# Kernel optimization log

Measured on AMD Instinct MI355X. Metric: run time of the kernel, lower is better.

## Reference

```python
import jax, jax.numpy as jnp
import numpy as np

N = 8192
IN_DIM = 512
HID = 512


def setup_inputs() -> dict:
    key = jax.random.key(0)
    k1, k2, k3, k4 = jax.random.split(key, 4)
    input_features = jax.random.normal(k1, (N, IN_DIM), dtype=jnp.float32)
    # positive weighted adjacency so degrees > 0
    adjacency_matrix = jax.random.uniform(k2, (N, N), dtype=jnp.float32)
    # xavier_init: normal with std = 1/sqrt(in_dim/2)
    Wgcn1 = jax.random.normal(k3, (IN_DIM, HID), dtype=jnp.float32) * (1.0 / np.sqrt(IN_DIM / 2.0))
    bgcn1 = jnp.zeros((HID,), dtype=jnp.float32)
    Wgcn12 = jax.random.normal(k4, (HID, HID), dtype=jnp.float32) * (1.0 / np.sqrt(HID / 2.0))
    bgcn12 = jnp.zeros((HID,), dtype=jnp.float32)
    return {
        "input_features": input_features,
        "adjacency_matrix": adjacency_matrix,
        "Wgcn1": Wgcn1,
        "bgcn1": bgcn1,
        "Wgcn12": Wgcn12,
        "bgcn12": bgcn12,
    }


def reference(input_features, adjacency_matrix, Wgcn1, bgcn1, Wgcn12, bgcn12):
    # D^{-1/2} A D^{-1/2}: diag matmuls expressed as row/col elementwise scaling
    # (mathematically identical to torch.matmul(diag(d), A @ diag(d)))
    d_inv_sqrt = jnp.power(adjacency_matrix.sum(axis=1), -0.5)  # [N]
    norm_adj = d_inv_sqrt[:, None] * adjacency_matrix * d_inv_sqrt[None, :]  # [N, N]

    support = input_features @ Wgcn1            # [N, HID]
    out = norm_adj @ support + bgcn1            # [N, HID]
    out = jax.nn.relu(out)                      # dropout p=0.0 -> identity
    support = out @ Wgcn12                      # [N, HID]
    out = norm_adj @ support + bgcn12           # [N, HID]
    return out
```

## Files before the change

### kernel.cpp

```cpp
#include <hip/hip_runtime.h>
#include <stdint.h>


typedef __attribute__((ext_vector_type(8))) __bf16 bf16x8;
typedef __attribute__((ext_vector_type(4))) float f32x4;
typedef __attribute__((ext_vector_type(8))) unsigned short u16x8;

__device__ __forceinline__ unsigned short f2bf(float f) {
  union { float f; uint32_t u; } v; v.f = f;
  uint32_t u = v.u;
  return (unsigned short)((u + 0x7fffu + ((u >> 16) & 1u)) >> 16);
}

__device__ __forceinline__ float bf2f(unsigned short u) {
  union { uint32_t u; float f; } v; v.u = ((uint32_t)u) << 16; return v.f;
}

__device__ __forceinline__ void async_cp16(const void* g, void* lds) {
  auto gp = (const __attribute__((address_space(1))) uint32_t*)g;
  auto lp = (__attribute__((address_space(3))) uint32_t*)lds;
  __builtin_amdgcn_global_load_lds(gp, lp, 16, 0, 0);
}

__global__ __launch_bounds__(256) void k_rowsum_convert(
    const float* __restrict__ A, unsigned short* __restrict__ Abf,
    float* __restrict__ dvec, int ncols) {
  const int row = blockIdx.x;
  const float* arow = A + (size_t)row * ncols;
  unsigned short* orow = Abf + (size_t)row * ncols;
  float s = 0.f;
  for (int c = threadIdx.x * 4; c < ncols; c += 256 * 4) {
    float4 v = *(const float4*)(arow + c);
    s += (v.x + v.y) + (v.z + v.w);
    ushort4 o;
    o.x = f2bf(v.x); o.y = f2bf(v.y); o.z = f2bf(v.z); o.w = f2bf(v.w);
    *(ushort4*)(orow + c) = o;
  }
  #pragma unroll
  for (int off = 32; off > 0; off >>= 1) s += __shfl_down(s, off);
  __shared__ float red[4];
  if ((threadIdx.x & 63) == 0) red[threadIdx.x >> 6] = s;
  __syncthreads();
  if (threadIdx.x == 0) {
    float t = (red[0] + red[1]) + (red[2] + red[3]);
    dvec[row] = 1.0f / sqrtf(t);
  }
}

__global__ __launch_bounds__(256) void k_f32_to_bf16(
    const float* __restrict__ in, unsigned short* __restrict__ out, int n4) {
  int i = blockIdx.x * 256 + threadIdx.x;
  if (i < n4) {
    float4 v = ((const float4*)in)[i];
    ushort4 o;
    o.x = f2bf(v.x); o.y = f2bf(v.y); o.z = f2bf(v.z); o.w = f2bf(v.w);
    ((ushort4*)out)[i] = o;
  }
}

__global__ __launch_bounds__(256) void k_transpose_bf16(
    const float* __restrict__ in, unsigned short* __restrict__ out, int dim) {
  int o = blockIdx.x * 256 + threadIdx.x;
  if (o < dim * dim) {
    int k = o % dim;
    int n = o / dim;
    out[o] = f2bf(in[k * dim + n]);
  }
}

template <int MODE>
__global__ __launch_bounds__(256, 2) void gemm_bt(
    const unsigned short* __restrict__ Aop,
    const unsigned short* __restrict__ Bt,
    void* __restrict__ Cout,
    const float* __restrict__ dvec,
    const float* __restrict__ bias,
    int M, int N, int K) {
  constexpr int BM = 128, BN = 64, BK = 32;
  __shared__ unsigned short As[BM * BK];
  __shared__ unsigned short Bs[BN * BK];

  const int tid = threadIdx.x;
  const int w = tid >> 6;
  const int l = tid & 63;
  const int rowBase = blockIdx.y * BM;
  const int colBase = blockIdx.x * BN;
  const int waveM = w >> 1;
  const int waveN = w & 1;

  f32x4 acc[4][2];
  const f32x4 fz = {0.f, 0.f, 0.f, 0.f};
  #pragma unroll
  for (int m = 0; m < 4; ++m)
    #pragma unroll
    for (int n = 0; n < 2; ++n) acc[m][n] = fz;

  const int chunkRow = l >> 2;
  const int kOff = (l & 3) * 8;
  const unsigned short* gA0 = Aop + (size_t)(rowBase + w * 16 + chunkRow) * K + kOff;
  const unsigned short* gA1 = gA0 + (size_t)64 * K;
  const unsigned short* gB0 = Bt + (size_t)(colBase + w * 16 + chunkRow) * K + kOff;
  unsigned short* lA0 = As + w * 512;
  unsigned short* lA1 = As + (w + 4) * 512;
  unsigned short* lB0 = Bs + w * 512;

  const int kfrag = (l >> 4) * 8;
  const int lrow = l & 15;

  for (int k0 = 0; k0 < K; k0 += BK) {
    async_cp16(gA0 + k0, lA0);
    async_cp16(gA1 + k0, lA1);
    async_cp16(gB0 + k0, lB0);
    __syncthreads();

    bf16x8 af[4], bfr[2];
    #pragma unroll
    for (int m = 0; m < 4; ++m)
      af[m] = *(const bf16x8*)(As + (waveM * 64 + m * 16 + lrow) * BK + kfrag);
    #pragma unroll
    for (int n = 0; n < 2; ++n)
      bfr[n] = *(const bf16x8*)(Bs + (waveN * 32 + n * 16 + lrow) * BK + kfrag);

    #pragma unroll
    for (int m = 0; m < 4; ++m)
      #pragma unroll
      for (int n = 0; n < 2; ++n)
        acc[m][n] = __builtin_amdgcn_mfma_f32_16x16x32_bf16(af[m], bfr[n],
                                                            acc[m][n], 0, 0, 0);
    __syncthreads();
  }

  const int erow0 = rowBase + waveM * 64 + (l >> 4) * 4;
  const int ecol0 = colBase + waveN * 32 + (l & 15);
  #pragma unroll
  for (int m = 0; m < 4; ++m) {
    #pragma unroll
    for (int n = 0; n < 2; ++n) {
      #pragma unroll
      for (int j = 0; j < 4; ++j) {
        const int rowg = erow0 + m * 16 + j;
        const int colg = ecol0 + n * 16;
        float v = acc[m][n][j];
        if (MODE == 0) {
          v *= dvec[colg];
          ((unsigned short*)Cout)[(size_t)rowg * N + colg] = f2bf(v);
        }
      }
    }
  }
}

__global__ __launch_bounds__(256, 2) void gemm_big2(
    const unsigned short* __restrict__ Aop,
    const unsigned short* __restrict__ Bt,
    unsigned short* __restrict__ Pout,
    int M, int N, int K, int kLen) {
  constexpr int BK = 32;
  constexpr int BUF = 24576;
  __shared__ char lds[3 * BUF];

  const int tid = threadIdx.x;
  const int w = tid >> 6;
  const int l = tid & 63;

  const int id = blockIdx.x;
  const int q = id & 7, s = id >> 3;
  const int bx = s & 3;
  const int by = ((q & 1) << 4) | (s >> 2);
  const int bz = q >> 1;

  const int rowBase = by * 256;
  const int colBase = bx * 128;
  const int kBase = bz * kLen;
  const int waveM = w >> 1;
  const int waveN = w & 1;

  f32x4 acc[8][4];
  const f32x4 fz = {0.f, 0.f, 0.f, 0.f};
  #pragma unroll
  for (int m = 0; m < 8; ++m)
    #pragma unroll
    for (int n = 0; n < 4; ++n) acc[m][n] = fz;

  const int srcElem = ((l & 3) ^ ((l >> 3) & 3)) * 8;
  const unsigned short* aSrc =
      Aop + (size_t)(rowBase + w * 64 + (l >> 2)) * K + kBase + srcElem;
  const unsigned short* bSrc =
      Bt + (size_t)(colBase + w * 32 + (l >> 2)) * K + kBase + srcElem;
  const int dstA = w * 4096 + l * 16;
  const int dstB = 16384 + w * 2048 + l * 16;

#define STAGE_A(tt, bb)                                                   \
  {                                                                       \
    const size_t o = (size_t)(tt) * BK;                                   \
    async_cp16(aSrc + o, lds + (bb) + dstA);                              \
    async_cp16(aSrc + (size_t)16 * K + o, lds + (bb) + dstA + 1024);      \
    async_cp16(aSrc + (size_t)32 * K + o, lds + (bb) + dstA + 2048);      \
    async_cp16(aSrc + (size_t)48 * K + o, lds + (bb) + dstA + 3072);      \
  }
#define STAGE_B(tt, bb)                                                   \
  {                                                                       \
    const size_t o = (size_t)(tt) * BK;                                   \
    async_cp16(bSrc + o, lds + (bb) + dstB);                              \
    async_cp16(bSrc + (size_t)16 * K + o, lds + (bb) + dstB + 1024);      \
  }

  const int nt = kLen / BK;
  STAGE_A(0, 0); STAGE_B(0, 0);
  STAGE_A(1, BUF); STAGE_B(1, BUF);

  const int lrow = l & 15;
  const int kq = l >> 4;
  const int xr = (lrow >> 1) & 3;
  const int slotByte = ((kq ^ xr) << 4);
  const int aRow0 = (waveM * 128 + lrow) * 64;
  const int bRow0 = 16384 + (waveN * 64 + lrow) * 64;

  int cur = 0, nxt = BUF, fut = 2 * BUF;
  for (int t = 0; t < nt; ++t) {
    if (t == nt - 1) {
      asm volatile("s_waitcnt vmcnt(0)" ::: "memory");
    } else {
      asm volatile("s_waitcnt vmcnt(6)" ::: "memory");
    }
    __builtin_amdgcn_s_barrier();

    bf16x8 af[4], bfr[4];
    #pragma unroll
    for (int i = 0; i < 4; ++i)
      af[i] = *(const bf16x8*)(lds + cur + aRow0 + i * 16 * 64 + slotByte);
    #pragma unroll
    for (int n = 0; n < 4; ++n)
      bfr[n] = *(const bf16x8*)(lds + cur + bRow0 + n * 16 * 64 + slotByte);
    if (t + 2 < nt) STAGE_A(t + 2, fut);
    __builtin_amdgcn_s_barrier();
    __builtin_amdgcn_s_setprio(1);
    #pragma unroll
    for (int i = 0; i < 4; ++i)
      #pragma unroll
      for (int n = 0; n < 4; ++n)
        acc[i][n] = __builtin_amdgcn_mfma_f32_16x16x32_bf16(
            af[i], bfr[n], acc[i][n], 0, 0, 0);
    __builtin_amdgcn_s_setprio(0);

    bf16x8 af2[4];
    #pragma unroll
    for (int i = 0; i < 4; ++i)
      af2[i] = *(const bf16x8*)(lds + cur + aRow0 + (64 + i * 16) * 64 + slotByte);
    if (t + 2 < nt) STAGE_B(t + 2, fut);
    __builtin_amdgcn_s_barrier();
    __builtin_amdgcn_s_setprio(1);
    #pragma unroll
    for (int i = 0; i < 4; ++i)
      #pragma unroll
      for (int n = 0; n < 4; ++n)
        acc[4 + i][n] = __builtin_amdgcn_mfma_f32_16x16x32_bf16(
            af2[i], bfr[n], acc[4 + i][n], 0, 0, 0);
    __builtin_amdgcn_s_setprio(0);

    const int tmp = cur; cur = nxt; nxt = fut; fut = tmp;
  }
#undef STAGE_A
#undef STAGE_B

  unsigned short* pz = Pout + (size_t)bz * M * N;
  const int erow0 = rowBase + waveM * 128 + (l >> 4) * 4;
  const int ecol0 = colBase + waveN * 64 + (l & 15);
  #pragma unroll
  for (int m = 0; m < 8; ++m) {
    #pragma unroll
    for (int n = 0; n < 4; ++n) {
      #pragma unroll
      for (int j = 0; j < 4; ++j) {
        pz[(size_t)(erow0 + m * 16 + j) * N + ecol0 + n * 16] =
            f2bf(acc[m][n][j]);
      }
    }
  }
}

template <int MODE>
__global__ __launch_bounds__(256) void k_reduce(
    const unsigned short* __restrict__ parts,
    const float* __restrict__ dvec,
    const float* __restrict__ bias,
    void* __restrict__ outp, int M, int N) {
  const size_t MN = (size_t)M * N;
  const size_t idx = ((size_t)blockIdx.x * 256 + threadIdx.x) * 8;
  if (idx >= MN) return;
  const int row = (int)(idx / N);
  const int col = (int)(idx % N);
  const float di = dvec[row];
  float s[8] = {0, 0, 0, 0, 0, 0, 0, 0};
  #pragma unroll
  for (int z = 0; z < 4; ++z) {
    u16x8 v = *(const u16x8*)(parts + z * MN + idx);
    #pragma unroll
    for (int e = 0; e < 8; ++e) s[e] += bf2f(v[e]);
  }
  if (MODE == 1) {
    ushort4 o0, o1;
    unsigned short tmp[8];
    #pragma unroll
    for (int e = 0; e < 8; ++e) {
      float v = di * s[e] + bias[col + e];
      v = v > 0.f ? v : 0.f;
      tmp[e] = f2bf(v);
    }
    o0.x = tmp[0]; o0.y = tmp[1]; o0.z = tmp[2]; o0.w = tmp[3];
    o1.x = tmp[4]; o1.y = tmp[5]; o1.z = tmp[6]; o1.w = tmp[7];
    *(ushort4*)((unsigned short*)outp + idx) = o0;
    *(ushort4*)((unsigned short*)outp + idx + 4) = o1;
  } else {
    float4 o0, o1;
    o0.x = di * s[0] + bias[col + 0];
    o0.y = di * s[1] + bias[col + 1];
    o0.z = di * s[2] + bias[col + 2];
    o0.w = di * s[3] + bias[col + 3];
    o1.x = di * s[4] + bias[col + 4];
    o1.y = di * s[5] + bias[col + 5];
    o1.z = di * s[6] + bias[col + 6];
    o1.w = di * s[7] + bias[col + 7];
    *(float4*)((float*)outp + idx) = o0;
    *(float4*)((float*)outp + idx + 4) = o1;
  }
}

extern "C" void kernel_launch(void* const* d_in, const int* in_sizes, int n_in,
                              void* d_out, int out_size, void* d_ws, size_t ws_size,
                              hipStream_t stream) {
  const float* X  = (const float*)d_in[0];
  const float* A  = (const float*)d_in[1];
  const float* W1 = (const float*)d_in[2];
  const float* b1 = (const float*)d_in[3];
  const float* W2 = (const float*)d_in[4];
  const float* b2 = (const float*)d_in[5];
  float* out = (float*)d_out;

  constexpr int NN = 8192, IN = 512, HID = 512;
  constexpr int KSPLIT = 4;

  char* ws = (char*)d_ws;
  float* ddeg = (float*)ws;
  unsigned short* Abf = (unsigned short*)(ws + (32 << 10));
  unsigned short* W1t = Abf + (size_t)NN * NN;
  unsigned short* W2t = W1t + IN * HID;
  unsigned short* P0  = W2t + HID * HID;
  unsigned short* P1  = P0 + (size_t)NN * HID;
  unsigned short* parts = P1 + (size_t)NN * HID;

  k_rowsum_convert<<<NN, 256, 0, stream>>>(A, Abf, ddeg, NN);
  k_f32_to_bf16<<<(NN * IN / 4 + 255) / 256, 256, 0, stream>>>(X, P0, NN * IN / 4);
  k_transpose_bf16<<<(IN * HID + 255) / 256, 256, 0, stream>>>(W1, W1t, IN);
  k_transpose_bf16<<<(HID * HID + 255) / 256, 256, 0, stream>>>(W2, W2t, HID);

  gemm_bt<0><<<dim3(NN / 64, HID / 128), 256, 0, stream>>>(
      W1t, P0, P1, ddeg, nullptr, HID, NN, IN);
  gemm_big2<<<4 * (NN / 256) * KSPLIT, 256, 0, stream>>>(
      Abf, P1, parts, NN, HID, NN, NN / KSPLIT);
  k_reduce<1><<<(int)((size_t)NN * HID / 8 / 256), 256, 0, stream>>>(
      parts, ddeg, b1, P0, NN, HID);
  gemm_bt<0><<<dim3(NN / 64, HID / 128), 256, 0, stream>>>(
      W2t, P0, P1, ddeg, nullptr, HID, NN, HID);
  gemm_big2<<<4 * (NN / 256) * KSPLIT, 256, 0, stream>>>(
      Abf, P1, parts, NN, HID, NN, NN / KSPLIT);
  k_reduce<2><<<(int)((size_t)NN * HID / 8 / 256), 256, 0, stream>>>(
      parts, ddeg, b2, out, NN, HID);
}
```

Measured before the change: 278.5 us.

## Enlarge big GEMM tile to 256x256 and drop mid-loop barriers

The large adjacency GEMM moves from 256x128 block tiles to 256x256 tiles, so each wave computes 128x128 with 64 accumulators. This halves the number of times the A operand (the 8192x8192 adjacency) is streamed from memory and doubles arithmetic per LDS load. The inner loop is restructured to interleave fragment loads with four MFMA quadrants, and the intermediate barriers and priority hints are removed. In exchange it needs one block per CU with heavy register use, launches half as many blocks (256 on a GPU with 256 CUs), and removing barriers risks the async stage for t+2 overwriting a buffer that slower waves still read.

```diff
diff --git a/kernel.cpp b/kernel.cpp
--- a/kernel.cpp
+++ b/kernel.cpp
@@ -150,13 +150,13 @@
   }
 }
 
-__global__ __launch_bounds__(256, 2) void gemm_big2(
+__global__ __launch_bounds__(256, 1) void gemm_big4(
     const unsigned short* __restrict__ Aop,
     const unsigned short* __restrict__ Bt,
     unsigned short* __restrict__ Pout,
     int M, int N, int K, int kLen) {
   constexpr int BK = 32;
-  constexpr int BUF = 24576;
+  constexpr int BUF = 32768;
   __shared__ char lds[3 * BUF];
 
   const int tid = threadIdx.x;
@@ -165,30 +165,30 @@
 
   const int id = blockIdx.x;
   const int q = id & 7, s = id >> 3;
-  const int bx = s & 3;
-  const int by = ((q & 1) << 4) | (s >> 2);
+  const int bx = s & 1;
+  const int by = ((q & 1) << 4) | (s >> 1);
   const int bz = q >> 1;
 
   const int rowBase = by * 256;
-  const int colBase = bx * 128;
+  const int colBase = bx * 256;
   const int kBase = bz * kLen;
-  const int waveM = w >> 1;
-  const int waveN = w & 1;
-
-  f32x4 acc[8][4];
+  const int wm = w >> 1;
+  const int wn = w & 1;
+
+  f32x4 acc[8][8];
   const f32x4 fz = {0.f, 0.f, 0.f, 0.f};
   #pragma unroll
   for (int m = 0; m < 8; ++m)
     #pragma unroll
-    for (int n = 0; n < 4; ++n) acc[m][n] = fz;
+    for (int n = 0; n < 8; ++n) acc[m][n] = fz;
 
   const int srcElem = ((l & 3) ^ ((l >> 3) & 3)) * 8;
   const unsigned short* aSrc =
       Aop + (size_t)(rowBase + w * 64 + (l >> 2)) * K + kBase + srcElem;
   const unsigned short* bSrc =
-      Bt + (size_t)(colBase + w * 32 + (l >> 2)) * K + kBase + srcElem;
+      Bt + (size_t)(colBase + w * 64 + (l >> 2)) * K + kBase + srcElem;
   const int dstA = w * 4096 + l * 16;
-  const int dstB = 16384 + w * 2048 + l * 16;
+  const int dstB = 16384 + w * 4096 + l * 16;
 
 #define STAGE_A(tt, bb)                                                   \
   {                                                                       \
@@ -203,6 +203,8 @@
     const size_t o = (size_t)(tt) * BK;                                   \
     async_cp16(bSrc + o, lds + (bb) + dstB);                              \
     async_cp16(bSrc + (size_t)16 * K + o, lds + (bb) + dstB + 1024);      \
+    async_cp16(bSrc + (size_t)32 * K + o, lds + (bb) + dstB + 2048);      \
+    async_cp16(bSrc + (size_t)48 * K + o, lds + (bb) + dstB + 3072);      \
   }
 
   const int nt = kLen / BK;
@@ -213,50 +215,64 @@
   const int kq = l >> 4;
   const int xr = (lrow >> 1) & 3;
   const int slotByte = ((kq ^ xr) << 4);
-  const int aRow0 = (waveM * 128 + lrow) * 64;
-  const int bRow0 = 16384 + (waveN * 64 + lrow) * 64;
+  const int aRow0 = (wm * 128 + lrow) * 64;
+  const int bRow0 = 16384 + (wn * 128 + lrow) * 64;
 
   int cur = 0, nxt = BUF, fut = 2 * BUF;
   for (int t = 0; t < nt; ++t) {
     if (t == nt - 1) {
       asm volatile("s_waitcnt vmcnt(0)" ::: "memory");
     } else {
-      asm volatile("s_waitcnt vmcnt(6)" ::: "memory");
+      asm volatile("s_waitcnt vmcnt(8)" ::: "memory");
     }
     __builtin_amdgcn_s_barrier();
 
-    bf16x8 af[4], bfr[4];
+    bf16x8 A0[4], A1[4], B0[4], B1[4];
     #pragma unroll
     for (int i = 0; i < 4; ++i)
-      af[i] = *(const bf16x8*)(lds + cur + aRow0 + i * 16 * 64 + slotByte);
-    #pragma unroll
-    for (int n = 0; n < 4; ++n)
-      bfr[n] = *(const bf16x8*)(lds + cur + bRow0 + n * 16 * 64 + slotByte);
+      A0[i] = *(const bf16x8*)(lds + cur + aRow0 + i * 1024 + slotByte);
+    #pragma unroll
+    for (int i = 0; i < 4; ++i)
+      B0[i] = *(const bf16x8*)(lds + cur + bRow0 + i * 1024 + slotByte);
+    #pragma unroll
+    for (int i = 0; i < 4; ++i)
+      B1[i] = *(const bf16x8*)(lds + cur + bRow0 + (4 + i) * 1024 + slotByte);
+
+    #pragma unroll
+    for (int m = 0; m < 4; ++m)
+      #pragma unroll
+      for (int n = 0; n < 4; ++n)
+        acc[m][n] = __builtin_amdgcn_mfma_f32_16x16x32_bf16(
+            A0[m], B0[n], acc[m][n], 0, 0, 0);
+
+    #pragma unroll
+    for (int i = 0; i < 4; ++i)
+      A1[i] = *(const bf16x8*)(lds + cur + aRow0 + (4 + i) * 1024 + slotByte);
+
+    #pragma unroll
+    for (int m = 0; m < 4; ++m)
+      #pragma unroll
+      for (int n = 0; n < 4; ++n)
+        acc[m][4 + n] = __builtin_amdgcn_mfma_f32_16x16x32_bf16(
+            A0[m], B1[n], acc[m][4 + n], 0, 0, 0);
+
     if (t + 2 < nt) STAGE_A(t + 2, fut);
-    __builtin_amdgcn_s_barrier();
-    __builtin_amdgcn_s_setprio(1);
-    #pragma unroll
-    for (int i = 0; i < 4; ++i)
+
+    #pragma unroll
+    for (int m = 0; m < 4; ++m)
       #pragma unroll
       for (int n = 0; n < 4; ++n)
-        acc[i][n] = __builtin_amdgcn_mfma_f32_16x16x32_bf16(
-            af[i], bfr[n], acc[i][n], 0, 0, 0);
-    __builtin_amdgcn_s_setprio(0);
-
-    bf16x8 af2[4];
-    #pragma unroll
-    for (int i = 0; i < 4; ++i)
-      af2[i] = *(const bf16x8*)(lds + cur + aRow0 + (64 + i * 16) * 64 + slotByte);
+        acc[4 + m][n] = __builtin_amdgcn_mfma_f32_16x16x32_bf16(
+            A1[m], B0[n], acc[4 + m][n], 0, 0, 0);
+
     if (t + 2 < nt) STAGE_B(t + 2, fut);
-    __builtin_amdgcn_s_barrier();
-    __builtin_amdgcn_s_setprio(1);
-    #pragma unroll
-    for (int i = 0; i < 4; ++i)
+
+    #pragma unroll
+    for (int m = 0; m < 4; ++m)
       #pragma unroll
       for (int n = 0; n < 4; ++n)
-        acc[4 + i][n] = __builtin_amdgcn_mfma_f32_16x16x32_bf16(
-            af2[i], bfr[n], acc[4 + i][n], 0, 0, 0);
-    __builtin_amdgcn_s_setprio(0);
+        acc[4 + m][4 + n] = __builtin_amdgcn_mfma_f32_16x16x32_bf16(
+            A1[m], B1[n], acc[4 + m][4 + n], 0, 0, 0);
 
     const int tmp = cur; cur = nxt; nxt = fut; fut = tmp;
   }
@@ -264,12 +280,12 @@
 #undef STAGE_B
 
   unsigned short* pz = Pout + (size_t)bz * M * N;
-  const int erow0 = rowBase + waveM * 128 + (l >> 4) * 4;
-  const int ecol0 = colBase + waveN * 64 + (l & 15);
+  const int erow0 = rowBase + wm * 128 + (l >> 4) * 4;
+  const int ecol0 = colBase + wn * 128 + (l & 15);
   #pragma unroll
   for (int m = 0; m < 8; ++m) {
     #pragma unroll
-    for (int n = 0; n < 4; ++n) {
+    for (int n = 0; n < 8; ++n) {
       #pragma unroll
       for (int j = 0; j < 4; ++j) {
         pz[(size_t)(erow0 + m * 16 + j) * N + ecol0 + n * 16] =
@@ -356,13 +372,13 @@
 
   gemm_bt<0><<<dim3(NN / 64, HID / 128), 256, 0, stream>>>(
       W1t, P0, P1, ddeg, nullptr, HID, NN, IN);
-  gemm_big2<<<4 * (NN / 256) * KSPLIT, 256, 0, stream>>>(
+  gemm_big4<<<2 * (NN / 256) * KSPLIT, 256, 0, stream>>>(
       Abf, P1, parts, NN, HID, NN, NN / KSPLIT);
   k_reduce<1><<<(int)((size_t)NN * HID / 8 / 256), 256, 0, stream>>>(
       parts, ddeg, b1, P0, NN, HID);
   gemm_bt<0><<<dim3(NN / 64, HID / 128), 256, 0, stream>>>(
       W2t, P0, P1, ddeg, nullptr, HID, NN, HID);
-  gemm_big2<<<4 * (NN / 256) * KSPLIT, 256, 0, stream>>>(
+  gemm_big4<<<2 * (NN / 256) * KSPLIT, 256, 0, stream>>>(
       Abf, P1, parts, NN, HID, NN, NN / KSPLIT);
   k_reduce<2><<<(int)((size_t)NN * HID / 8 / 256), 256, 0, stream>>>(
       parts, ddeg, b2, out, NN, HID);
```

Result: faster. 268.0 us (-3.8%).
